# Performance work log

Measured on AMD Instinct MI355X. Metric: run time of the kernel, lower is better.

The kernel has to match this reference:

```python
import jax, jax.numpy as jnp
import numpy as np

H, DH = 8, 32            # heads, per-head dim
F_DIM = H * DH           # hidden_channels = 256
N_P, N_A = 100000, 50000 # paper / author node counts
E_AP, E_PA, E_PP = 300000, 300000, 500000
N_CLASSES = 32


def _seg_softmax(alpha, idx, n):
    # softmax over edges grouped by destination node (per head)
    m = jax.ops.segment_max(alpha, idx, num_segments=n)
    m = jnp.where(jnp.isfinite(m), m, 0.0)  # nodes with no in-edges
    e = jnp.exp(alpha - m[idx])
    s = jax.ops.segment_sum(e, idx, num_segments=n)
    return e / (s[idx] + 1e-16)


def _edge_attn(h_src, h_dst, a_src, a_dst, src, dst, n_dst):
    # h_*: [N, H, DH]; a_*: [H, DH]; src/dst: [E]
    als = jnp.einsum('nhd,hd->nh', h_src, a_src)
    ald = jnp.einsum('nhd,hd->nh', h_dst, a_dst)
    alpha = jax.nn.leaky_relu(als[src] + ald[dst], negative_slope=0.2)  # [E,H]
    a = _seg_softmax(alpha, dst, n_dst)
    out = jax.ops.segment_sum(h_src[src] * a[:, :, None], dst, num_segments=n_dst)
    return jax.nn.relu(out).reshape(n_dst, F_DIM)


def _semantic(xs, kW, kb, q):
    # semantic (edge-type level) attention, PyG HANConv 'group'
    X = jnp.stack(xs)  # [K, N, F]
    score = jnp.einsum('f,kf->k', q, jnp.tanh(X @ kW + kb).mean(axis=1))
    attn = jax.nn.softmax(score)
    return jnp.einsum('k,knf->nf', attn, X)


def _han_layer(xP, xA, prm, edg):
    (W_P, b_P, W_A, b_A, aS_AP, aD_AP, aS_PA, aD_PA, aS_PP, aD_PP, kW, kb, q) = prm
    sAP, dAP, sPA, dPA, sPP, dPP = edg
    hP = (xP @ W_P + b_P).reshape(-1, H, DH)
    hA = (xA @ W_A + b_A).reshape(-1, H, DH)
    oAP = _edge_attn(hA, hP, aS_AP, aD_AP, sAP, dAP, N_P)  # author->paper
    oPP = _edge_attn(hP, hP, aS_PP, aD_PP, sPP, dPP, N_P)  # paper->paper
    oPA = _edge_attn(hP, hA, aS_PA, aD_PA, sPA, dPA, N_A)  # paper->author
    newP = _semantic([oAP, oPP], kW, kb, q)
    newA = _semantic([oPA], kW, kb, q)
    return newP, newA


def setup_inputs() -> dict:
    ks = iter(jax.random.split(jax.random.key(0), 80))
    def nrm(shape, scale=1.0):
        return jax.random.normal(next(ks), shape, dtype=jnp.float32) * scale
    def idx(n, high):
        return jax.random.randint(next(ks), (n,), 0, high, dtype=jnp.int32)
    inp = {}
    inp['x_P'] = nrm((N_P, 512))
    inp['x_A'] = nrm((N_A, 256))
    inp['src_AP'] = idx(E_AP, N_A); inp['dst_AP'] = idx(E_AP, N_P)
    inp['src_PA'] = idx(E_PA, N_P); inp['dst_PA'] = idx(E_PA, N_A)
    inp['src_PP'] = idx(E_PP, N_P); inp['dst_PP'] = idx(E_PP, N_P)
    for l, inP, inA in ((0, 512, 256), (1, F_DIM, F_DIM)):
        inp[f'W{l}_P'] = nrm((inP, F_DIM), 0.05)
        inp[f'b{l}_P'] = jnp.zeros((F_DIM,), jnp.float32)
        inp[f'W{l}_A'] = nrm((inA, F_DIM), 0.05)
        inp[f'b{l}_A'] = jnp.zeros((F_DIM,), jnp.float32)
        for et in ('AP', 'PA', 'PP'):
            inp[f'as{l}_{et}'] = nrm((H, DH), 0.1)
            inp[f'ad{l}_{et}'] = nrm((H, DH), 0.1)
        inp[f'k{l}_W'] = nrm((F_DIM, F_DIM), 0.05)
        inp[f'k{l}_b'] = jnp.zeros((F_DIM,), jnp.float32)
        inp[f'q{l}'] = nrm((F_DIM,), 0.1)
    inp['lin_W'] = nrm((F_DIM, N_CLASSES), 0.05)
    inp['lin_b'] = jnp.zeros((N_CLASSES,), jnp.float32)
    return inp


def reference(x_P, x_A, src_AP, dst_AP, src_PA, dst_PA, src_PP, dst_PP,
              W0_P, b0_P, W0_A, b0_A, as0_AP, ad0_AP, as0_PA, ad0_PA, as0_PP, ad0_PP, k0_W, k0_b, q0,
              W1_P, b1_P, W1_A, b1_A, as1_AP, ad1_AP, as1_PA, ad1_PA, as1_PP, ad1_PP, k1_W, k1_b, q1,
              lin_W, lin_b):
    edg = (src_AP, dst_AP, src_PA, dst_PA, src_PP, dst_PP)
    p0 = (W0_P, b0_P, W0_A, b0_A, as0_AP, ad0_AP, as0_PA, ad0_PA, as0_PP, ad0_PP, k0_W, k0_b, q0)
    p1 = (W1_P, b1_P, W1_A, b1_A, as1_AP, ad1_AP, as1_PA, ad1_PA, as1_PP, ad1_PP, k1_W, k1_b, q1)
    xP, xA = _han_layer(x_P, x_A, p0, edg)
    xP, xA = _han_layer(xP, xA, p1, edg)
    # final classifier on labeled_class = 'paper' (dropout is eval-mode no-op)
    return xP @ lin_W + lin_b
```

## Files before the change

### kernel.cpp

```cpp
#include <hip/hip_runtime.h>
#include <math.h>

typedef unsigned short u16;
typedef u16 ushort8 __attribute__((ext_vector_type(8)));
typedef __bf16 bf16x8 __attribute__((ext_vector_type(8)));
typedef float floatx4 __attribute__((ext_vector_type(4)));

__device__ __forceinline__ float bf2f(u16 u) {
  union { unsigned int i; float f; } v; v.i = ((unsigned int)u) << 16; return v.f;
}
__device__ __forceinline__ u16 f2bf(float f) {
  union { float f; unsigned int i; } v; v.f = f;
  return (u16)((v.i + 0x7fffu + ((v.i >> 16) & 1u)) >> 16);
}

#define CEILDIV(a, b) (((a) + (b) - 1) / (b))

typedef const __attribute__((address_space(1))) unsigned int ga_u32;
typedef __attribute__((address_space(3))) unsigned int lds_u32;
__device__ __forceinline__ void gload16(const u16* g, u16* l) {
  __builtin_amdgcn_global_load_lds((ga_u32*)g, (lds_u32*)l, 16, 0, 0);
}

__global__ void k_transpose(const float* __restrict__ W, u16* __restrict__ Wt, int K, int N) {
  int t = blockIdx.x * blockDim.x + threadIdx.x;
  if (t >= K * N) return;
  int n = t / K, k = t - n * K;
  Wt[t] = f2bf(W[k * N + n]);
}

__global__ void k_hist(const int* __restrict__ dst, int E, int* __restrict__ cnt) {
  int t = blockIdx.x * blockDim.x + threadIdx.x;
  if (t < E) atomicAdd(&cnt[dst[t]], 1);
}

__device__ __forceinline__ void seg_map(int b, int& seg, int& bs, int& n) {
  if (b < 98) { seg = 0; bs = b; n = 100000; }
  else if (b < 196) { seg = 1; bs = b - 98; n = 100000; }
  else { seg = 2; bs = b - 196; n = 50000; }
}

__global__ __launch_bounds__(256) void k_scan_a(
    const int* __restrict__ c0, const int* __restrict__ c1, const int* __restrict__ c2,
    int* __restrict__ bsum) {
  int seg, bs, n;
  seg_map(blockIdx.x, seg, bs, n);
  const int* cnt = seg == 0 ? c0 : (seg == 1 ? c1 : c2);
  int t = threadIdx.x;
  int base = bs * 1024 + t * 4;
  int s = 0;
#pragma unroll
  for (int j = 0; j < 4; j++) { int i = base + j; if (i < n) s += cnt[i]; }
#pragma unroll
  for (int o = 1; o < 64; o <<= 1) s += __shfl_xor(s, o);
  __shared__ int wt[4];
  int lane = t & 63, w = t >> 6;
  if (lane == 0) wt[w] = s;
  __syncthreads();
  if (t == 0) bsum[seg * 256 + bs] = wt[0] + wt[1] + wt[2] + wt[3];
}

__global__ __launch_bounds__(256) void k_scan_b(
    const int* __restrict__ bsum, int* __restrict__ bbase,
    int* __restrict__ rp0, int* __restrict__ rp1, int* __restrict__ rp2) {
  __shared__ int sm[256];
  int t = threadIdx.x;
  for (int seg = 0; seg < 3; ++seg) {
    int nb = (seg == 2) ? 49 : 98;
    int n = (seg == 2) ? 50000 : 100000;
    int v = (t < nb) ? bsum[seg * 256 + t] : 0;
    sm[t] = v;
    __syncthreads();
    for (int o = 1; o < 256; o <<= 1) {
      int u = (t >= o) ? sm[t - o] : 0;
      __syncthreads();
      sm[t] += u;
      __syncthreads();
    }
    if (t < nb) bbase[seg * 256 + t] = sm[t] - v;
    if (t == 255) {
      int* rp = seg == 0 ? rp0 : (seg == 1 ? rp1 : rp2);
      rp[n] = sm[255];
    }
    __syncthreads();
  }
}

__global__ __launch_bounds__(256) void k_scan_c(
    const int* __restrict__ c0, const int* __restrict__ c1, const int* __restrict__ c2,
    const int* __restrict__ bbase,
    int* __restrict__ rp0, int* __restrict__ rp1, int* __restrict__ rp2) {
  int seg, bs, n;
  seg_map(blockIdx.x, seg, bs, n);
  const int* cnt = seg == 0 ? c0 : (seg == 1 ? c1 : c2);
  int* rp = seg == 0 ? rp0 : (seg == 1 ? rp1 : rp2);
  int t = threadIdx.x;
  int base = bs * 1024 + t * 4;
  int c[4];
  int s = 0;
#pragma unroll
  for (int j = 0; j < 4; j++) { int i = base + j; c[j] = (i < n) ? cnt[i] : 0; s += c[j]; }
  int lane = t & 63, w = t >> 6;
  int incl = s;
#pragma unroll
  for (int o = 1; o < 64; o <<= 1) { int u = __shfl_up(incl, o); if (lane >= o) incl += u; }
  __shared__ int wt[4];
  if (lane == 63) wt[w] = incl;
  __syncthreads();
  int wb = 0;
#pragma unroll
  for (int j = 0; j < 4; j++) if (j < w) wb += wt[j];
  int thr = bbase[seg * 256 + bs] + wb + incl - s;
#pragma unroll
  for (int j = 0; j < 4; j++) { int i = base + j; if (i < n) rp[i] = thr; thr += c[j]; }
}

__global__ void k_scatter(const int* __restrict__ dst, const int* __restrict__ src, int E,
                          const int* __restrict__ rp, int* __restrict__ cur,
                          int* __restrict__ esrc) {
  int t = blockIdx.x * blockDim.x + threadIdx.x;
  if (t >= E) return;
  int d = dst[t];
  int p = atomicAdd(&cur[d], 1);
  esrc[rp[d] + p] = src[t];
}

#define G3_BM 128
#define G3_BN 256
#define G3_BK 32

template <int SRC, int MODE>
__global__ __launch_bounds__(512) void k_gemm3(
    const void* __restrict__ Av, const u16* __restrict__ A2, const float* __restrict__ attn,
    const u16* __restrict__ Bt, const float* __restrict__ bias,
    u16* __restrict__ Cb, float* __restrict__ colsum, int M, int K) {
  __shared__ __align__(16) u16 sm[2][(G3_BM + G3_BN) * G3_BK];
  int tid = threadIdx.x;
  int lane = tid & 63, wid = tid >> 6;
  int wm = wid >> 2, wn = wid & 3;
  int quad = lane >> 4, l16 = lane & 15;
  int m0 = blockIdx.x * G3_BM;

  float a0s = 0.f, a1s = 0.f;
  if (SRC == 1) { a0s = attn[0]; a1s = attn[1]; }

  int gr_ = tid >> 2;
  int gc_ = (tid & 3) * 8;
  int arow = m0 + gr_; if (arow >= M) arow = M - 1;
  const u16* gaB = (SRC != 2) ? (const u16*)Av + (size_t)arow * K + gc_ : nullptr;
  const u16* ga2 = (SRC == 1) ? A2 + (size_t)arow * K + gc_ : nullptr;
  const float* gaF = (SRC == 2) ? (const float*)Av + (size_t)arow * K + gc_ : nullptr;
  const u16* gb0 = Bt + (size_t)gr_ * K + gc_;
  const u16* gb1 = Bt + (size_t)(128 + gr_) * K + gc_;
  const int laA = wid * 512;
  const int laB0 = 4096 + wid * 512;
  const int laB1 = 8192 + wid * 512;

  floatx4 acc[4][4];
#pragma unroll
  for (int i = 0; i < 4; i++)
#pragma unroll
    for (int j = 0; j < 4; j++) acc[i][j] = (floatx4){0.f, 0.f, 0.f, 0.f};

  auto stage = [&](int buf, int k0) {
    u16* sa = sm[buf];
    if (SRC == 0) {
      gload16(gaB + k0, sa + laA);
    } else if (SRC == 2) {
      const floatx4* p = (const floatx4*)(gaF + k0);
      floatx4 v0 = p[0], v1 = p[1];
      u16 t[8];
#pragma unroll
      for (int j = 0; j < 4; j++) { t[j] = f2bf(v0[j]); t[4 + j] = f2bf(v1[j]); }
      *(ushort8*)(sa + laA + (lane << 3)) = *(ushort8*)t;
    } else {
      ushort8 u = *(const ushort8*)(gaB + k0);
      ushort8 w = *(const ushort8*)(ga2 + k0);
      u16 t[8];
#pragma unroll
      for (int j = 0; j < 8; j++) t[j] = f2bf(a0s * bf2f(u[j]) + a1s * bf2f(w[j]));
      *(ushort8*)(sa + laA + (lane << 3)) = *(ushort8*)t;
    }
    gload16(gb0 + k0, sa + laB0);
    gload16(gb1 + k0, sa + laB1);
  };

  stage(0, 0);
  __syncthreads();

  int nk = K / G3_BK;
  for (int t = 0; t < nk; ++t) {
    int cur = t & 1;
    if (t + 1 < nk) stage(cur ^ 1, (t + 1) * G3_BK);
    const u16* Ab = sm[cur];
    const u16* Bb = sm[cur] + G3_BM * G3_BK;
    bf16x8 af[4], bfr[4];
#pragma unroll
    for (int mi = 0; mi < 4; mi++)
      af[mi] = *(const bf16x8*)(Ab + (wm * 64 + mi * 16 + l16) * G3_BK + quad * 8);
#pragma unroll
    for (int ni = 0; ni < 4; ni++)
      bfr[ni] = *(const bf16x8*)(Bb + (wn * 64 + ni * 16 + l16) * G3_BK + quad * 8);
#pragma unroll
    for (int mi = 0; mi < 4; mi++)
#pragma unroll
      for (int ni = 0; ni < 4; ni++)
        acc[mi][ni] = __builtin_amdgcn_mfma_f32_16x16x32_bf16(af[mi], bfr[ni], acc[mi][ni], 0, 0, 0);
    __syncthreads();
  }

  if (MODE == 1) {
#pragma unroll
    for (int ni = 0; ni < 4; ni++) {
      int gc = wn * 64 + ni * 16 + l16;
      float bv = bias[gc];
      float part = 0.f;
#pragma unroll
      for (int mi = 0; mi < 4; mi++) {
#pragma unroll
        for (int r = 0; r < 4; r++) {
          int gr = m0 + wm * 64 + mi * 16 + quad * 4 + r;
          if (gr < M) {
            float v = acc[mi][ni][r] + bv;
            float e2 = __expf(2.f * v);
            part += 1.f - 2.f / (e2 + 1.f);
          }
        }
      }
      part += __shfl_xor(part, 16);
      part += __shfl_xor(part, 32);
      if (lane < 16) atomicAdd(&colsum[gc], part);
    }
  } else {
    float* smf = (float*)sm;
    float* tw = smf + wid * 16 * 68;
#pragma unroll
    for (int mi = 0; mi < 4; mi++) {
#pragma unroll
      for (int ni = 0; ni < 4; ni++)
#pragma unroll
        for (int r = 0; r < 4; r++)
          tw[(quad * 4 + r) * 68 + ni * 16 + l16] = acc[mi][ni][r];
      int row = lane >> 2, cq = (lane & 3) * 16;
      int gr = m0 + wm * 64 + mi * 16 + row;
      if (gr < M) {
        int gc0 = wn * 64 + cq;
        u16 ob[16];
#pragma unroll
        for (int j = 0; j < 16; j++) ob[j] = f2bf(tw[row * 68 + cq + j] + bias[gc0 + j]);
        *(ushort8*)(Cb + (size_t)gr * 256 + gc0) = *(ushort8*)ob;
        *(ushort8*)(Cb + (size_t)gr * 256 + gc0 + 8) = *(ushort8*)(ob + 8);
      }
    }
  }
}

#define BM 128
#define BN 128
#define BK 32

__global__ __launch_bounds__(256) void k_gemm2_cls(
    const u16* __restrict__ A, const u16* __restrict__ A2, const float* __restrict__ attn,
    const u16* __restrict__ Bt, const float* __restrict__ bias,
    float* __restrict__ Cf, int M, int N, int K) {
  __shared__ __align__(16) u16 sm[2][2][BM * BK];
  int tid = threadIdx.x;
  int lane = tid & 63, wid = tid >> 6;
  int wm = wid >> 1, wn = wid & 1;
  int quad = lane >> 4, l16 = lane & 15;
  int m0 = blockIdx.x * BM, n0 = 0;

  float a0s = attn[0], a1s = attn[1];

  int sr = lane >> 2;
  int sc = (lane & 3) * 8;
  int ra0 = m0 + wid * 32 + sr;
  int ra1 = ra0 + 16;
  int rb0 = n0 + wid * 32 + sr;
  int rb1 = rb0 + 16;
  if (ra0 >= M) ra0 = M - 1;
  if (ra1 >= M) ra1 = M - 1;
  if (rb0 >= N) rb0 = N - 1;
  if (rb1 >= N) rb1 = N - 1;
  const u16* ga0 = A + (size_t)ra0 * K + sc;
  const u16* ga1 = A + (size_t)ra1 * K + sc;
  const u16* g2a0 = A2 + (size_t)ra0 * K + sc;
  const u16* g2a1 = A2 + (size_t)ra1 * K + sc;
  const u16* gb0 = Bt + (size_t)rb0 * K + sc;
  const u16* gb1 = Bt + (size_t)rb1 * K + sc;
  const int la = wid * 32 * BK;
  const int lb = la + 16 * BK;

  floatx4 acc[4][4];
#pragma unroll
  for (int i = 0; i < 4; i++)
#pragma unroll
    for (int j = 0; j < 4; j++) acc[i][j] = (floatx4){0.f, 0.f, 0.f, 0.f};

  auto stage = [&](int buf, int k0) {
    u16* sa = &sm[buf][0][0];
    u16* sb = &sm[buf][1][0];
    ushort8 u0 = *(const ushort8*)(ga0 + k0);
    ushort8 w0 = *(const ushort8*)(g2a0 + k0);
    ushort8 u1 = *(const ushort8*)(ga1 + k0);
    ushort8 w1 = *(const ushort8*)(g2a1 + k0);
    u16 t0[8], t1[8];
#pragma unroll
    for (int j = 0; j < 8; j++) {
      t0[j] = f2bf(a0s * bf2f(u0[j]) + a1s * bf2f(w0[j]));
      t1[j] = f2bf(a0s * bf2f(u1[j]) + a1s * bf2f(w1[j]));
    }
    *(ushort8*)(sa + la + lane * 8) = *(ushort8*)t0;
    *(ushort8*)(sa + lb + lane * 8) = *(ushort8*)t1;
    gload16(gb0 + k0, sb + la);
    gload16(gb1 + k0, sb + lb);
  };

  stage(0, 0);
  __syncthreads();

  int nk = K / BK;
  for (int t = 0; t < nk; ++t) {
    int cur = t & 1;
    if (t + 1 < nk) stage(cur ^ 1, (t + 1) * BK);
    const u16* Ab = &sm[cur][0][0];
    const u16* Bb = &sm[cur][1][0];
    bf16x8 af[4], bfr[4];
#pragma unroll
    for (int mi = 0; mi < 4; mi++)
      af[mi] = *(const bf16x8*)(Ab + (wm * 64 + mi * 16 + l16) * BK + quad * 8);
#pragma unroll
    for (int ni = 0; ni < 4; ni++)
      bfr[ni] = *(const bf16x8*)(Bb + (wn * 64 + ni * 16 + l16) * BK + quad * 8);
#pragma unroll
    for (int mi = 0; mi < 4; mi++)
#pragma unroll
      for (int ni = 0; ni < 4; ni++)
        acc[mi][ni] = __builtin_amdgcn_mfma_f32_16x16x32_bf16(af[mi], bfr[ni], acc[mi][ni], 0, 0, 0);
    __syncthreads();
  }

#pragma unroll
  for (int ni = 0; ni < 4; ni++) {
    int gc = n0 + wn * 64 + ni * 16 + l16;
    if (gc >= N) continue;
    float bv = bias[gc];
#pragma unroll
    for (int mi = 0; mi < 4; mi++) {
#pragma unroll
      for (int r = 0; r < 4; r++) {
        int gr = m0 + wm * 64 + mi * 16 + quad * 4 + r;
        if (gr < M) Cf[(size_t)gr * N + gc] = acc[mi][ni][r] + bv;
      }
    }
  }
}

__global__ void k_logits(const u16* __restrict__ h, int N,
                         const float* __restrict__ a0, const float* __restrict__ a1,
                         const float* __restrict__ a2, const float* __restrict__ a3,
                         float* __restrict__ o0, float* __restrict__ o1,
                         float* __restrict__ o2, float* __restrict__ o3) {
  int t = blockIdx.x * blockDim.x + threadIdx.x;
  int n = t >> 3, hh = t & 7;
  if (n >= N) return;
  const ushort8* hp = (const ushort8*)(h + (size_t)n * 256 + hh * 32);
  float d0 = 0.f, d1 = 0.f, d2 = 0.f, d3 = 0.f;
#pragma unroll
  for (int q = 0; q < 4; q++) {
    ushort8 v = hp[q];
#pragma unroll
    for (int j = 0; j < 8; j++) {
      float f = bf2f(v[j]);
      int idx = hh * 32 + q * 8 + j;
      d0 += f * a0[idx];
      d1 += f * a1[idx];
      if (a2) d2 += f * a2[idx];
      if (a3) d3 += f * a3[idx];
    }
  }
  o0[t] = d0;
  o1[t] = d1;
  if (o2) o2[t] = d2;
  if (o3) o3[t] = d3;
}

__global__ __launch_bounds__(256) void k_attn_agg(
    const int* __restrict__ rp, const int* __restrict__ esrc,
    const float* __restrict__ als, const float* __restrict__ ald,
    const u16* __restrict__ hsrc, u16* __restrict__ out, int Ndst) {
  int wid = threadIdx.x >> 6, lane = threadIdx.x & 63;
  int n = blockIdx.x * 4 + wid;
  if (n >= Ndst) return;
  int hh = lane >> 3;
  int b = rp[n], e = rp[n + 1];
  float av = ald[n * 8 + hh];
  float m = -1e30f, s = 0.f;
  float a0 = 0.f, a1 = 0.f, a2 = 0.f, a3 = 0.f;
  int i = b;
  for (; i + 1 < e; i += 2) {
    int s0 = esrc[i], s1 = esrc[i + 1];
    float x0 = als[s0 * 8 + hh] + av, x1 = als[s1 * 8 + hh] + av;
    ushort4 v0 = *(const ushort4*)(hsrc + (size_t)s0 * 256 + lane * 4);
    ushort4 v1 = *(const ushort4*)(hsrc + (size_t)s1 * 256 + lane * 4);
    x0 = x0 > 0.f ? x0 : 0.2f * x0;
    x1 = x1 > 0.f ? x1 : 0.2f * x1;
    float mx = fmaxf(x0, x1);
    if (mx > m) {
      float r = __expf(m - mx);
      s *= r; a0 *= r; a1 *= r; a2 *= r; a3 *= r;
      m = mx;
    }
    float w0 = __expf(x0 - m), w1 = __expf(x1 - m);
    s += w0 + w1;
    a0 += w0 * bf2f(v0.x) + w1 * bf2f(v1.x);
    a1 += w0 * bf2f(v0.y) + w1 * bf2f(v1.y);
    a2 += w0 * bf2f(v0.z) + w1 * bf2f(v1.z);
    a3 += w0 * bf2f(v0.w) + w1 * bf2f(v1.w);
  }
  if (i < e) {
    int s0 = esrc[i];
    float x0 = als[s0 * 8 + hh] + av;
    ushort4 v0 = *(const ushort4*)(hsrc + (size_t)s0 * 256 + lane * 4);
    x0 = x0 > 0.f ? x0 : 0.2f * x0;
    if (x0 > m) {
      float r = __expf(m - x0);
      s *= r; a0 *= r; a1 *= r; a2 *= r; a3 *= r;
      m = x0;
    }
    float w0 = __expf(x0 - m);
    s += w0;
    a0 += w0 * bf2f(v0.x);
    a1 += w0 * bf2f(v0.y);
    a2 += w0 * bf2f(v0.z);
    a3 += w0 * bf2f(v0.w);
  }
  float inv = 1.f / (s + 1e-16f);
  a0 *= inv; a1 *= inv; a2 *= inv; a3 *= inv;
  ushort4 o;
  o.x = f2bf(a0 > 0.f ? a0 : 0.f);
  o.y = f2bf(a1 > 0.f ? a1 : 0.f);
  o.z = f2bf(a2 > 0.f ? a2 : 0.f);
  o.w = f2bf(a3 > 0.f ? a3 : 0.f);
  *(ushort4*)(out + (size_t)n * 256 + lane * 4) = o;
}

__global__ void k_scores(const float* __restrict__ cs0, const float* __restrict__ cs1,
                         const float* __restrict__ q, float invN, float* __restrict__ attn) {
  int lane = threadIdx.x;
  float p0 = 0.f, p1 = 0.f;
  for (int f = lane; f < 256; f += 64) {
    float qv = q[f];
    p0 += qv * cs0[f];
    p1 += qv * cs1[f];
  }
  for (int o = 32; o > 0; o >>= 1) {
    p0 += __shfl_down(p0, o);
    p1 += __shfl_down(p1, o);
  }
  if (lane == 0) {
    float s0 = p0 * invN, s1 = p1 * invN;
    float mx = fmaxf(s0, s1);
    float e0 = __expf(s0 - mx), e1 = __expf(s1 - mx);
    float den = e0 + e1;
    attn[0] = e0 / den;
    attn[1] = e1 / den;
  }
}

extern "C" void kernel_launch(void* const* d_in, const int* in_sizes, int n_in,
                              void* d_out, int out_size, void* d_ws, size_t ws_size,
                              hipStream_t stream) {
  const int NP = 100000, NA = 50000;
  const int EAP = 300000, EPA = 300000, EPP = 500000;

  const float* xP = (const float*)d_in[0];
  const float* xA = (const float*)d_in[1];
  const int* srcAP = (const int*)d_in[2];
  const int* dstAP = (const int*)d_in[3];
  const int* srcPA = (const int*)d_in[4];
  const int* dstPA = (const int*)d_in[5];
  const int* srcPP = (const int*)d_in[6];
  const int* dstPP = (const int*)d_in[7];
  const float *W_P[2], *b_P[2], *W_A[2], *b_A[2];
  const float *asAP[2], *adAP[2], *asPA[2], *adPA[2], *asPP[2], *adPP[2];
  const float *kW[2], *kb[2], *qv[2];
  for (int l = 0; l < 2; ++l) {
    int base = 8 + l * 13;
    W_P[l] = (const float*)d_in[base + 0];
    b_P[l] = (const float*)d_in[base + 1];
    W_A[l] = (const float*)d_in[base + 2];
    b_A[l] = (const float*)d_in[base + 3];
    asAP[l] = (const float*)d_in[base + 4];
    adAP[l] = (const float*)d_in[base + 5];
    asPA[l] = (const float*)d_in[base + 6];
    adPA[l] = (const float*)d_in[base + 7];
    asPP[l] = (const float*)d_in[base + 8];
    adPP[l] = (const float*)d_in[base + 9];
    kW[l] = (const float*)d_in[base + 10];
    kb[l] = (const float*)d_in[base + 11];
    qv[l] = (const float*)d_in[base + 12];
  }
  const float* linW = (const float*)d_in[34];
  const float* linb = (const float*)d_in[35];

  char* ws = (char*)d_ws;
  size_t off = 0;
  auto alloc = [&](size_t bytes) -> char* {
    char* p = ws + off;
    off += (bytes + 255) & ~(size_t)255;
    return p;
  };
  u16* P1 = (u16*)alloc((size_t)NP * 256 * 2);
  u16* P2 = (u16*)alloc((size_t)NP * 256 * 2);
  u16* A1 = (u16*)alloc((size_t)NA * 256 * 2);
  u16* A2 = (u16*)alloc((size_t)NA * 256 * 2);
  u16* P3 = (u16*)alloc((size_t)NP * 256 * 2);
  float* ldAP_P = (float*)alloc((size_t)NP * 8 * 4);
  float* lsPA_P = (float*)alloc((size_t)NP * 8 * 4);
  float* lsPP_P = (float*)alloc((size_t)NP * 8 * 4);
  float* ldPP_P = (float*)alloc((size_t)NP * 8 * 4);
  float* lsAP_A = (float*)alloc((size_t)NA * 8 * 4);
  float* ldPA_A = (float*)alloc((size_t)NA * 8 * 4);
  u16* wtP0 = (u16*)alloc(256 * 512 * 2);
  u16* wtA0 = (u16*)alloc(256 * 256 * 2);
  u16* wtP1 = (u16*)alloc(256 * 256 * 2);
  u16* wtA1 = (u16*)alloc(256 * 256 * 2);
  u16* kwt0 = (u16*)alloc(256 * 256 * 2);
  u16* kwt1 = (u16*)alloc(256 * 256 * 2);
  u16* lwt = (u16*)alloc(32 * 256 * 2);
  int* rpAP = (int*)alloc((NP + 1) * 4);
  int* rpPP = (int*)alloc((NP + 1) * 4);
  int* rpPA = (int*)alloc((NA + 1) * 4);
  int* eiAP = (int*)alloc((size_t)EAP * 4);
  int* eiPP = (int*)alloc((size_t)EPP * 4);
  int* eiPA = (int*)alloc((size_t)EPA * 4);
  int* bsum = (int*)alloc(768 * 4);
  int* bbase = (int*)alloc(768 * 4);
  size_t zbytes = (size_t)(4 * NP + 2 * NA) * 4 + 4 * 256 * 4;
  char* zblock = alloc(zbytes);
  int* cntAP = (int*)zblock;
  int* cntPP = cntAP + NP;
  int* cntPA = cntPP + NP;
  int* curAP = cntPA + NA;
  int* curPP = curAP + NP;
  int* curPA = curPP + NP;
  float* cs = (float*)(curPA + NA);
  float* attnBuf = (float*)alloc(256);

  u16* HP = A1;
  u16* hA0 = P2;
  u16* P2b = P2 + (size_t)NA * 256;

  (void)hipMemsetAsync((void*)zblock, 0, zbytes, stream);

  k_transpose<<<CEILDIV(512 * 256, 256), 256, 0, stream>>>(W_P[0], wtP0, 512, 256);
  k_transpose<<<CEILDIV(256 * 256, 256), 256, 0, stream>>>(W_A[0], wtA0, 256, 256);
  k_transpose<<<CEILDIV(256 * 256, 256), 256, 0, stream>>>(W_P[1], wtP1, 256, 256);
  k_transpose<<<CEILDIV(256 * 256, 256), 256, 0, stream>>>(W_A[1], wtA1, 256, 256);
  k_transpose<<<CEILDIV(256 * 256, 256), 256, 0, stream>>>(kW[0], kwt0, 256, 256);
  k_transpose<<<CEILDIV(256 * 256, 256), 256, 0, stream>>>(kW[1], kwt1, 256, 256);
  k_transpose<<<CEILDIV(256 * 32, 256), 256, 0, stream>>>(linW, lwt, 256, 32);

  k_hist<<<CEILDIV(EAP, 256), 256, 0, stream>>>(dstAP, EAP, cntAP);
  k_hist<<<CEILDIV(EPP, 256), 256, 0, stream>>>(dstPP, EPP, cntPP);
  k_hist<<<CEILDIV(EPA, 256), 256, 0, stream>>>(dstPA, EPA, cntPA);
  k_scan_a<<<245, 256, 0, stream>>>(cntAP, cntPP, cntPA, bsum);
  k_scan_b<<<1, 256, 0, stream>>>(bsum, bbase, rpAP, rpPP, rpPA);
  k_scan_c<<<245, 256, 0, stream>>>(cntAP, cntPP, cntPA, bbase, rpAP, rpPP, rpPA);
  k_scatter<<<CEILDIV(EAP, 256), 256, 0, stream>>>(dstAP, srcAP, EAP, rpAP, curAP, eiAP);
  k_scatter<<<CEILDIV(EPP, 256), 256, 0, stream>>>(dstPP, srcPP, EPP, rpPP, curPP, eiPP);
  k_scatter<<<CEILDIV(EPA, 256), 256, 0, stream>>>(dstPA, srcPA, EPA, rpPA, curPA, eiPA);

  int gP = CEILDIV(NP, G3_BM), gA = CEILDIV(NA, G3_BM);

  k_gemm3<2, 0><<<gP, 512, 0, stream>>>(xP, nullptr, nullptr, wtP0, b_P[0], HP, nullptr, NP, 512);
  k_gemm3<2, 0><<<gA, 512, 0, stream>>>(xA, nullptr, nullptr, wtA0, b_A[0], hA0, nullptr, NA, 256);

  k_logits<<<CEILDIV(NP * 8, 256), 256, 0, stream>>>(
      HP, NP, adAP[0], asPA[0], asPP[0], adPP[0], ldAP_P, lsPA_P, lsPP_P, ldPP_P);
  k_logits<<<CEILDIV(NA * 8, 256), 256, 0, stream>>>(
      hA0, NA, asAP[0], adPA[0], nullptr, nullptr, lsAP_A, ldPA_A, nullptr, nullptr);
  k_attn_agg<<<CEILDIV(NP, 4), 256, 0, stream>>>(rpPP, eiPP, lsPP_P, ldPP_P, HP, P1, NP);
  k_attn_agg<<<CEILDIV(NA, 4), 256, 0, stream>>>(rpPA, eiPA, lsPA_P, ldPA_A, HP, P2b, NA);
  k_attn_agg<<<CEILDIV(NP, 4), 256, 0, stream>>>(rpAP, eiAP, lsAP_A, ldAP_P, hA0, HP, NP);
  k_gemm3<0, 1><<<gP, 512, 0, stream>>>(HP, nullptr, nullptr, kwt0, kb[0], nullptr, cs, NP, 256);
  k_gemm3<0, 1><<<gP, 512, 0, stream>>>(P1, nullptr, nullptr, kwt0, kb[0], nullptr, cs + 256, NP, 256);
  k_scores<<<1, 64, 0, stream>>>(cs, cs + 256, qv[0], 1.0f / NP, attnBuf);
  k_gemm3<1, 0><<<gP, 512, 0, stream>>>(HP, P1, attnBuf, wtP1, b_P[1], P3, nullptr, NP, 256);

  k_gemm3<0, 0><<<gA, 512, 0, stream>>>(P2b, nullptr, nullptr, wtA1, b_A[1], hA0, nullptr, NA, 256);
  k_logits<<<CEILDIV(NP * 8, 256), 256, 0, stream>>>(
      P3, NP, adAP[1], asPA[1], asPP[1], adPP[1], ldAP_P, lsPA_P, lsPP_P, ldPP_P);
  k_logits<<<CEILDIV(NA * 8, 256), 256, 0, stream>>>(
      hA0, NA, asAP[1], adPA[1], nullptr, nullptr, lsAP_A, ldPA_A, nullptr, nullptr);
  k_attn_agg<<<CEILDIV(NP, 4), 256, 0, stream>>>(rpPP, eiPP, lsPP_P, ldPP_P, P3, P1, NP);
  k_attn_agg<<<CEILDIV(NP, 4), 256, 0, stream>>>(rpAP, eiAP, lsAP_A, ldAP_P, hA0, HP, NP);
  k_gemm3<0, 1><<<gP, 512, 0, stream>>>(HP, nullptr, nullptr, kwt1, kb[1], nullptr, cs + 512, NP, 256);
  k_gemm3<0, 1><<<gP, 512, 0, stream>>>(P1, nullptr, nullptr, kwt1, kb[1], nullptr, cs + 768, NP, 256);
  k_scores<<<1, 64, 0, stream>>>(cs + 512, cs + 768, qv[1], 1.0f / NP, attnBuf + 2);

  k_gemm2_cls<<<CEILDIV(NP, BM), 256, 0, stream>>>(
      HP, P1, attnBuf + 2, lwt, linb, (float*)d_out, NP, 32, 256);
}
```

Before: 1.380 ms.

## Fuse histogram and scatter launches, unroll attention aggregation by four, cap GEMM occupancy

Merges the three per-edge-type histogram and scatter kernels into single launches that split threads across edge types, reducing launch count and tail underutilization. Unrolls the online-softmax aggregation loop from two to four edges per step to put more independent gathers in flight. Adds a minimum-blocks hint to the GEMM launch bounds, which may force register spilling. The three changes are independent of each other.

Result: no change. 1.370 ms (-0.8%).

```diff
diff --git a/kernel.cpp b/kernel.cpp
--- a/kernel.cpp
+++ b/kernel.cpp
@@ -29,9 +29,38 @@
   Wt[t] = f2bf(W[k * N + n]);
 }
 
-__global__ void k_hist(const int* __restrict__ dst, int E, int* __restrict__ cnt) {
+__global__ void k_hist3(const int* __restrict__ d0, int E0, int* __restrict__ c0,
+                        const int* __restrict__ d1, int E1, int* __restrict__ c1,
+                        const int* __restrict__ d2, int E2, int* __restrict__ c2) {
   int t = blockIdx.x * blockDim.x + threadIdx.x;
-  if (t < E) atomicAdd(&cnt[dst[t]], 1);
+  if (t < E0) atomicAdd(&c0[d0[t]], 1);
+  else if (t < E0 + E1) atomicAdd(&c1[d1[t - E0]], 1);
+  else if (t < E0 + E1 + E2) atomicAdd(&c2[d2[t - E0 - E1]], 1);
+}
+
+__global__ void k_scatter3(
+    const int* __restrict__ d0, const int* __restrict__ s0v, int E0,
+    const int* __restrict__ rp0, int* __restrict__ cur0, int* __restrict__ es0,
+    const int* __restrict__ d1, const int* __restrict__ s1v, int E1,
+    const int* __restrict__ rp1, int* __restrict__ cur1, int* __restrict__ es1,
+    const int* __restrict__ d2, const int* __restrict__ s2v, int E2,
+    const int* __restrict__ rp2, int* __restrict__ cur2, int* __restrict__ es2) {
+  int t = blockIdx.x * blockDim.x + threadIdx.x;
+  if (t < E0) {
+    int d = d0[t];
+    int p = atomicAdd(&cur0[d], 1);
+    es0[rp0[d] + p] = s0v[t];
+  } else if (t < E0 + E1) {
+    int u = t - E0;
+    int d = d1[u];
+    int p = atomicAdd(&cur1[d], 1);
+    es1[rp1[d] + p] = s1v[u];
+  } else if (t < E0 + E1 + E2) {
+    int u = t - E0 - E1;
+    int d = d2[u];
+    int p = atomicAdd(&cur2[d], 1);
+    es2[rp2[d] + p] = s2v[u];
+  }
 }
 
 __device__ __forceinline__ void seg_map(int b, int& seg, int& bs, int& n) {
@@ -115,22 +144,12 @@
   for (int j = 0; j < 4; j++) { int i = base + j; if (i < n) rp[i] = thr; thr += c[j]; }
 }
 
-__global__ void k_scatter(const int* __restrict__ dst, const int* __restrict__ src, int E,
-                          const int* __restrict__ rp, int* __restrict__ cur,
-                          int* __restrict__ esrc) {
-  int t = blockIdx.x * blockDim.x + threadIdx.x;
-  if (t >= E) return;
-  int d = dst[t];
-  int p = atomicAdd(&cur[d], 1);
-  esrc[rp[d] + p] = src[t];
-}
-
 #define G3_BM 128
 #define G3_BN 256
 #define G3_BK 32
 
 template <int SRC, int MODE>
-__global__ __launch_bounds__(512) void k_gemm3(
+__global__ __launch_bounds__(512, 4) void k_gemm3(
     const void* __restrict__ Av, const u16* __restrict__ A2, const float* __restrict__ attn,
     const u16* __restrict__ Bt, const float* __restrict__ bias,
     u16* __restrict__ Cb, float* __restrict__ colsum, int M, int K) {
@@ -398,27 +417,33 @@
   float m = -1e30f, s = 0.f;
   float a0 = 0.f, a1 = 0.f, a2 = 0.f, a3 = 0.f;
   int i = b;
-  for (; i + 1 < e; i += 2) {
-    int s0 = esrc[i], s1 = esrc[i + 1];
+  for (; i + 3 < e; i += 4) {
+    int s0 = esrc[i], s1 = esrc[i + 1], s2 = esrc[i + 2], s3 = esrc[i + 3];
     float x0 = als[s0 * 8 + hh] + av, x1 = als[s1 * 8 + hh] + av;
+    float x2 = als[s2 * 8 + hh] + av, x3 = als[s3 * 8 + hh] + av;
     ushort4 v0 = *(const ushort4*)(hsrc + (size_t)s0 * 256 + lane * 4);
     ushort4 v1 = *(const ushort4*)(hsrc + (size_t)s1 * 256 + lane * 4);
+    ushort4 v2 = *(const ushort4*)(hsrc + (size_t)s2 * 256 + lane * 4);
+    ushort4 v3 = *(const ushort4*)(hsrc + (size_t)s3 * 256 + lane * 4);
     x0 = x0 > 0.f ? x0 : 0.2f * x0;
     x1 = x1 > 0.f ? x1 : 0.2f * x1;
-    float mx = fmaxf(x0, x1);
+    x2 = x2 > 0.f ? x2 : 0.2f * x2;
+    x3 = x3 > 0.f ? x3 : 0.2f * x3;
+    float mx = fmaxf(fmaxf(x0, x1), fmaxf(x2, x3));
     if (mx > m) {
       float r = __expf(m - mx);
       s *= r; a0 *= r; a1 *= r; a2 *= r; a3 *= r;
       m = mx;
     }
     float w0 = __expf(x0 - m), w1 = __expf(x1 - m);
-    s += w0 + w1;
-    a0 += w0 * bf2f(v0.x) + w1 * bf2f(v1.x);
-    a1 += w0 * bf2f(v0.y) + w1 * bf2f(v1.y);
-    a2 += w0 * bf2f(v0.z) + w1 * bf2f(v1.z);
-    a3 += w0 * bf2f(v0.w) + w1 * bf2f(v1.w);
-  }
-  if (i < e) {
+    float w2 = __expf(x2 - m), w3 = __expf(x3 - m);
+    s += (w0 + w1) + (w2 + w3);
+    a0 += w0 * bf2f(v0.x) + w1 * bf2f(v1.x) + w2 * bf2f(v2.x) + w3 * bf2f(v3.x);
+    a1 += w0 * bf2f(v0.y) + w1 * bf2f(v1.y) + w2 * bf2f(v2.y) + w3 * bf2f(v3.y);
+    a2 += w0 * bf2f(v0.z) + w1 * bf2f(v1.z) + w2 * bf2f(v2.z) + w3 * bf2f(v3.z);
+    a3 += w0 * bf2f(v0.w) + w1 * bf2f(v1.w) + w2 * bf2f(v2.w) + w3 * bf2f(v3.w);
+  }
+  for (; i < e; ++i) {
     int s0 = esrc[i];
     float x0 = als[s0 * 8 + hh] + av;
     ushort4 v0 = *(const ushort4*)(hsrc + (size_t)s0 * 256 + lane * 4);
@@ -562,15 +587,15 @@
   k_transpose<<<CEILDIV(256 * 256, 256), 256, 0, stream>>>(kW[1], kwt1, 256, 256);
   k_transpose<<<CEILDIV(256 * 32, 256), 256, 0, stream>>>(linW, lwt, 256, 32);
 
-  k_hist<<<CEILDIV(EAP, 256), 256, 0, stream>>>(dstAP, EAP, cntAP);
-  k_hist<<<CEILDIV(EPP, 256), 256, 0, stream>>>(dstPP, EPP, cntPP);
-  k_hist<<<CEILDIV(EPA, 256), 256, 0, stream>>>(dstPA, EPA, cntPA);
+  k_hist3<<<CEILDIV(EAP + EPP + EPA, 256), 256, 0, stream>>>(
+      dstAP, EAP, cntAP, dstPP, EPP, cntPP, dstPA, EPA, cntPA);
   k_scan_a<<<245, 256, 0, stream>>>(cntAP, cntPP, cntPA, bsum);
   k_scan_b<<<1, 256, 0, stream>>>(bsum, bbase, rpAP, rpPP, rpPA);
   k_scan_c<<<245, 256, 0, stream>>>(cntAP, cntPP, cntPA, bbase, rpAP, rpPP, rpPA);
-  k_scatter<<<CEILDIV(EAP, 256), 256, 0, stream>>>(dstAP, srcAP, EAP, rpAP, curAP, eiAP);
-  k_scatter<<<CEILDIV(EPP, 256), 256, 0, stream>>>(dstPP, srcPP, EPP, rpPP, curPP, eiPP);
-  k_scatter<<<CEILDIV(EPA, 256), 256, 0, stream>>>(dstPA, srcPA, EPA, rpPA, curPA, eiPA);
+  k_scatter3<<<CEILDIV(EAP + EPP + EPA, 256), 256, 0, stream>>>(
+      dstAP, srcAP, EAP, rpAP, curAP, eiAP,
+      dstPP, srcPP, EPP, rpPP, curPP, eiPP,
+      dstPA, srcPA, EPA, rpPA, curPA, eiPA);
 
   int gP = CEILDIV(NP, G3_BM), gA = CEILDIV(NA, G3_BM);
 
```
